# Kernel optimization log

Measured on AMD Instinct MI355X. Metric: run time of the kernel, lower is better.

The kernel has to match this reference:

```python
import jax, jax.numpy as jnp
import numpy as np

EPS = 1e-5
K = 3
N_TAP = K * K


def _bn(x, g, b, m, v):
    # eval-mode batchnorm over channel axis 1 of NCHW
    inv = g / jnp.sqrt(v + EPS)
    return x * inv[None, :, None, None] + (b - m * inv)[None, :, None, None]


def _silu(x):
    return x * jax.nn.sigmoid(x)


def _dcn(x, offset, mask, w, b, pad=1):
    """Modulated deformable conv (DCNv2), stride 1.
    x: [B,C,H,W], offset: [B,2n,H,W] ((dy,dx) per tap), mask: [B,n,H,W],
    w: [O,C,K,K], b: [O]."""
    B, C, H, W = x.shape
    O = w.shape[0]
    ky, kx = jnp.meshgrid(jnp.arange(K), jnp.arange(K), indexing='ij')
    ky = ky.reshape(N_TAP).astype(x.dtype)
    kx = kx.reshape(N_TAP).astype(x.dtype)
    off = offset.reshape(B, N_TAP, 2, H, W)
    base_y = jnp.arange(H, dtype=x.dtype)[None, None, :, None]
    base_x = jnp.arange(W, dtype=x.dtype)[None, None, None, :]
    # fractional sample positions [B,n,H,W]
    py = base_y - pad + ky[None, :, None, None] + off[:, :, 0]
    px = base_x - pad + kx[None, :, None, None] + off[:, :, 1]
    y0 = jnp.floor(py)
    x0 = jnp.floor(px)
    fy = py - y0
    fx = px - x0
    y0i = y0.astype(jnp.int32)
    x0i = x0.astype(jnp.int32)
    x_flat = x.reshape(B, C, 1, H * W)

    def corner(yi, xi, wgt):
        valid = (yi >= 0) & (yi < H) & (xi >= 0) & (xi < W)
        idx = (jnp.clip(yi, 0, H - 1) * W + jnp.clip(xi, 0, W - 1)).reshape(B, 1, N_TAP, H * W)
        v = jnp.take_along_axis(x_flat, idx, axis=-1)  # [B,C,n,HW]
        return v * (wgt * valid.astype(x.dtype)).reshape(B, 1, N_TAP, H * W)

    acc = corner(y0i, x0i, (1 - fy) * (1 - fx))
    acc = acc + corner(y0i, x0i + 1, (1 - fy) * fx)
    acc = acc + corner(y0i + 1, x0i, fy * (1 - fx))
    acc = acc + corner(y0i + 1, x0i + 1, fy * fx)
    val = acc.reshape(B, C, N_TAP, H, W) * mask[:, None]  # modulation
    out = jnp.einsum('bcnhw,ocn->bohw', val, w.reshape(O, C, N_TAP))
    return out + b[None, :, None, None]


def setup_inputs() -> dict:
    key = jax.random.key(0)
    ks = jax.random.split(key, 16)
    B, C1, H, W = 8, 256, 80, 80
    C2 = 256
    Ch = 128  # c_ = int(c2 * 0.5)
    d = {}
    d['x'] = jax.random.normal(ks[0], (B, C1, H, W), jnp.float32)
    # cv1: 1x1 conv (no bias) + BN
    d['cv1_w'] = jax.random.normal(ks[1], (Ch, C1), jnp.float32) * (1.0 / np.sqrt(C1))
    d['bn1_g'] = jax.random.uniform(ks[2], (Ch,), jnp.float32, 0.5, 1.5)
    d['bn1_b'] = jax.random.normal(ks[3], (Ch,), jnp.float32) * 0.1
    d['bn1_m'] = jax.random.normal(ks[4], (Ch,), jnp.float32) * 0.1
    d['bn1_v'] = jax.random.uniform(ks[5], (Ch,), jnp.float32, 0.5, 1.5)
    # offset/mask predictor 3x3 conv (small weights -> modest deformation)
    d['off_w'] = jax.random.normal(ks[6], (3 * N_TAP, Ch, K, K), jnp.float32) * 0.01
    d['off_b'] = jnp.zeros((3 * N_TAP,), jnp.float32)
    # dcn main weight/bias
    d['dcn_w'] = jax.random.normal(ks[7], (Ch, Ch, K, K), jnp.float32) * (1.0 / np.sqrt(Ch * N_TAP))
    d['dcn_b'] = jnp.zeros((Ch,), jnp.float32)
    d['bn2_g'] = jax.random.uniform(ks[8], (Ch,), jnp.float32, 0.5, 1.5)
    d['bn2_b'] = jax.random.normal(ks[9], (Ch,), jnp.float32) * 0.1
    d['bn2_m'] = jax.random.normal(ks[10], (Ch,), jnp.float32) * 0.1
    d['bn2_v'] = jax.random.uniform(ks[11], (Ch,), jnp.float32, 0.5, 1.5)
    # cv2: 1x1 conv (no bias) + BN
    d['cv2_w'] = jax.random.normal(ks[12], (C2, Ch), jnp.float32) * (1.0 / np.sqrt(Ch))
    d['bn3_g'] = jax.random.uniform(ks[13], (C2,), jnp.float32, 0.5, 1.5)
    d['bn3_b'] = jax.random.normal(ks[14], (C2,), jnp.float32) * 0.1
    d['bn3_m'] = jax.random.normal(ks[15], (C2,), jnp.float32) * 0.1
    d['bn3_v'] = jnp.ones((C2,), jnp.float32)
    return d


def reference(x, cv1_w, bn1_g, bn1_b, bn1_m, bn1_v,
              off_w, off_b, dcn_w, dcn_b, bn2_g, bn2_b, bn2_m, bn2_v,
              cv2_w, bn3_g, bn3_b, bn3_m, bn3_v):
    # cv1: 1x1 conv -> BN -> SiLU
    y = _silu(_bn(jnp.einsum('bchw,oc->bohw', x, cv1_w), bn1_g, bn1_b, bn1_m, bn1_v))
    # offset/mask predictor: 3x3 conv, pad 1
    raw = jax.lax.conv_general_dilated(
        y, off_w, window_strides=(1, 1), padding=((1, 1), (1, 1)),
        dimension_numbers=('NCHW', 'OIHW', 'NCHW')) + off_b[None, :, None, None]
    offset = raw[:, :2 * N_TAP]
    mask = jax.nn.sigmoid(raw[:, 2 * N_TAP:])
    # modulated deformable 3x3 conv -> BN -> SiLU
    y = _silu(_bn(_dcn(y, offset, mask, dcn_w, dcn_b), bn2_g, bn2_b, bn2_m, bn2_v))
    # cv2: 1x1 conv -> BN -> SiLU
    y = _silu(_bn(jnp.einsum('bchw,oc->bohw', y, cv2_w), bn3_g, bn3_b, bn3_m, bn3_v))
    return x + y  # shortcut (c1 == c2)
```

## Files before the change

kernel.cpp:

```cpp
#include <hip/hip_runtime.h>
#include <math.h>

#define HWSZ 6400
#define WIMG 80
#define HIMG 80
#define BEPS 1e-5f

typedef __attribute__((ext_vector_type(8))) short short8;
typedef __attribute__((ext_vector_type(4))) float f32x4;
typedef __attribute__((ext_vector_type(4))) unsigned u32x4;

__device__ __forceinline__ unsigned short f2b(float f) {
    unsigned u = __builtin_bit_cast(unsigned, f);
    u += 0x7fffu + ((u >> 16) & 1u);
    return (unsigned short)(u >> 16);
}
__device__ __forceinline__ float b2f(unsigned short h) {
    unsigned u = ((unsigned)h) << 16;
    return __builtin_bit_cast(float, u);
}
__device__ __forceinline__ float silu_f(float t) { return t / (1.f + __expf(-t)); }

__global__ __launch_bounds__(256) void k_prep(
    const float* __restrict__ cv1w, const float* __restrict__ g1, const float* __restrict__ b1,
    const float* __restrict__ m1, const float* __restrict__ v1,
    const float* __restrict__ offw, const float* __restrict__ offb,
    const float* __restrict__ dcnw, const float* __restrict__ dcnb,
    const float* __restrict__ g2, const float* __restrict__ b2,
    const float* __restrict__ m2, const float* __restrict__ v2,
    const float* __restrict__ cv2w, const float* __restrict__ g3, const float* __restrict__ b3,
    const float* __restrict__ m3, const float* __restrict__ v3,
    unsigned short* __restrict__ apk1, unsigned short* __restrict__ apko,
    unsigned short* __restrict__ apkd, unsigned short* __restrict__ apk2,
    float* __restrict__ bias1, float* __restrict__ biaso,
    float* __restrict__ bias2, float* __restrict__ bias3)
{
    int idx = blockIdx.x * 256 + threadIdx.x;
    if (idx < 32768) {
        int j = idx & 7, L = (idx >> 3) & 63, ks = (idx >> 9) & 7, mt = idx >> 12;
        int o = mt * 16 + (L & 15), k = ks * 32 + (L >> 4) * 8 + j;
        float inv = g1[o] * rsqrtf(v1[o] + BEPS);
        apk1[idx] = f2b(cv1w[o * 256 + k] * inv);
    } else if (idx < 69632) {
        int t = idx - 32768;
        int j = t & 7, L = (t >> 3) & 63;
        int mt = t / 18432, rem = t % 18432, ks = rem >> 9;
        int o = mt * 16 + (L & 15);
        int kp = ks * 32 + (L >> 4) * 8 + j;
        int n = kp >> 7, c = kp & 127;
        float wv = (o < 27) ? offw[(size_t)(o * 128 + c) * 9 + n] : 0.f;
        apko[t] = f2b(wv);
    } else if (idx < 217088) {
        int t = idx - 69632;
        int j = t & 7, L = (t >> 3) & 63;
        int mt = t / 18432, rem = t % 18432, ks = rem >> 9;
        int o = mt * 16 + (L & 15);
        int kp = ks * 32 + (L >> 4) * 8 + j;
        int n = kp >> 7, c = kp & 127;
        float inv = g2[o] * rsqrtf(v2[o] + BEPS);
        apkd[t] = f2b(dcnw[(size_t)(o * 128 + c) * 9 + n] * inv);
    } else if (idx < 249856) {
        int t = idx - 217088;
        int j = t & 7, L = (t >> 3) & 63, ks = (t >> 9) & 3, mt = t >> 11;
        int o = mt * 16 + (L & 15), k = ks * 32 + (L >> 4) * 8 + j;
        float inv = g3[o] * rsqrtf(v3[o] + BEPS);
        apk2[t] = f2b(cv2w[o * 128 + k] * inv);
    } else if (idx < 250395) {
        int t = idx - 249856;
        if (t < 128) { float inv = g1[t] * rsqrtf(v1[t] + BEPS); bias1[t] = b1[t] - m1[t] * inv; }
        else if (t < 155) { biaso[t - 128] = offb[t - 128]; }
        else if (t < 283) { int o = t - 155; float inv = g2[o] * rsqrtf(v2[o] + BEPS);
                            bias2[o] = dcnb[o] * inv + b2[o] - m2[o] * inv; }
        else { int o = t - 283; float inv = g3[o] * rsqrtf(v3[o] + BEPS); bias3[o] = b3[o] - m3[o] * inv; }
    }
}

__global__ __launch_bounds__(256) void k_cv1(
    const float* __restrict__ x, const unsigned short* __restrict__ apk1,
    const float* __restrict__ bias1, unsigned short* __restrict__ y1t)
{
    __shared__ __align__(16) unsigned short sB[20480];
    int blk = blockIdx.x;
    int b = blk / 100, pt = blk % 100;
    int p0 = pt * 64;
    int tid = threadIdx.x;
    int lane = tid & 63;
    int w = tid >> 6;
    {
        int px = lane, q = w;
        const float* xb = x + (size_t)b * 256 * HWSZ + p0 + px;
        for (int ks = 0; ks < 8; ++ks) {
            unsigned pk[4];
#pragma unroll
            for (int t = 0; t < 4; ++t) {
                float f0 = xb[(size_t)(ks * 32 + q * 8 + 2 * t) * HWSZ];
                float f1 = xb[(size_t)(ks * 32 + q * 8 + 2 * t + 1) * HWSZ];
                asm("v_cvt_pk_bf16_f32 %0, %1, %2" : "=v"(pk[t]) : "v"(f0), "v"(f1));
            }
            *(u32x4*)&sB[((ks * 4 + (px >> 4)) * 16 + (px & 15)) * 40 + q * 8] =
                (u32x4){pk[0], pk[1], pk[2], pk[3]};
        }
    }
    __syncthreads();
    int n16 = lane & 15, qd = lane >> 4;
    f32x4 acc[2][4];
#pragma unroll
    for (int mi = 0; mi < 2; ++mi)
#pragma unroll
        for (int nt = 0; nt < 4; ++nt) acc[mi][nt] = (f32x4){0.f, 0.f, 0.f, 0.f};
    for (int ks = 0; ks < 8; ++ks) {
        short8 bf[4];
#pragma unroll
        for (int nt = 0; nt < 4; ++nt)
            bf[nt] = *(const short8*)&sB[((ks * 4 + nt) * 16 + n16) * 40 + qd * 8];
#pragma unroll
        for (int mi = 0; mi < 2; ++mi) {
            int mt = w * 2 + mi;
            short8 af = *(const short8*)&apk1[(size_t)((mt * 8 + ks) * 64 + lane) * 8];
#pragma unroll
            for (int nt = 0; nt < 4; ++nt)
                acc[mi][nt] = __builtin_amdgcn_mfma_f32_16x16x32_bf16(af, bf[nt], acc[mi][nt], 0, 0, 0);
        }
    }
    __syncthreads();
#pragma unroll
    for (int mi = 0; mi < 2; ++mi)
#pragma unroll
        for (int nt = 0; nt < 4; ++nt)
#pragma unroll
            for (int r = 0; r < 4; ++r) {
                int o = w * 32 + mi * 16 + qd * 4 + r;
                float sv = silu_f(acc[mi][nt][r] + bias1[o]);
                sB[(nt * 16 + n16) * 136 + o] = f2b(sv);
            }
    __syncthreads();
    {
        int px = tid >> 2, qq = tid & 3;
        unsigned short* ytb = y1t + ((size_t)b * HWSZ + p0 + px) * 128;
#pragma unroll
        for (int seg = 0; seg < 4; ++seg) {
            short8 v = *(const short8*)&sB[px * 136 + qq * 32 + seg * 8];
            *(short8*)&ytb[qq * 32 + seg * 8] = v;
        }
    }
}

__global__ __launch_bounds__(256) void k_off(
    const unsigned short* __restrict__ y1t, const unsigned short* __restrict__ apko,
    const float* __restrict__ biaso, float* __restrict__ raw)
{
    __shared__ __align__(16) unsigned short sV[227 * 136];
    int blk = blockIdx.x;
    int b = blk / 100, pt = blk % 100;
    int p0 = pt * 64;
    int tid = threadIdx.x;
    const unsigned short* yb = y1t + (size_t)b * HWSZ * 128;
    for (int c = tid; c < 226 * 16; c += 256) {
        int row = c >> 4, col = c & 15;
        int sp = p0 - 81 + row;
        sp = min(max(sp, 0), HWSZ - 1);
        *(short8*)&sV[row * 136 + col * 8] = *(const short8*)&yb[(size_t)sp * 128 + col * 8];
    }
    if (tid < 16) {
        short8 z = {0, 0, 0, 0, 0, 0, 0, 0};
        *(short8*)&sV[226 * 136 + tid * 8] = z;
    }
    __syncthreads();

    int lane = tid & 63, w = tid >> 6;
    int n16 = lane & 15, qd = lane >> 4;
    int p = p0 + w * 16 + n16;
    int h = p / WIMG, wx = p % WIMG;
    f32x4 acc[2];
    acc[0] = (f32x4){0.f, 0.f, 0.f, 0.f};
    acc[1] = (f32x4){0.f, 0.f, 0.f, 0.f};
#pragma unroll
    for (int n = 0; n < 9; ++n) {
        int dh = n / 3 - 1, dw = n % 3 - 1;
        int hh = h + dh, ww = wx + dw;
        bool valid = ((unsigned)hh < HIMG) && ((unsigned)ww < WIMG);
        int row = valid ? (81 + w * 16 + n16 + dh * WIMG + dw) : 226;
        const unsigned short* rV = &sV[row * 136 + qd * 8];
#pragma unroll
        for (int s = 0; s < 4; ++s) {
            int ks = n * 4 + s;
            short8 bf = *(const short8*)&rV[s * 32];
#pragma unroll
            for (int mi = 0; mi < 2; ++mi) {
                short8 af = *(const short8*)&apko[(size_t)((mi * 36 + ks) * 64 + lane) * 8];
                acc[mi] = __builtin_amdgcn_mfma_f32_16x16x32_bf16(af, bf, acc[mi], 0, 0, 0);
            }
        }
    }
    float* rb = raw + (size_t)b * 27 * HWSZ + p0 + w * 16 + n16;
#pragma unroll
    for (int mi = 0; mi < 2; ++mi)
#pragma unroll
        for (int r = 0; r < 4; ++r) {
            int o = mi * 16 + qd * 4 + r;
            if (o < 27) {
                float t = acc[mi][r] + biaso[o];
                if (o >= 18) t = 1.f / (1.f + __expf(-t));
                rb[(size_t)o * HWSZ] = t;
            }
        }
}

#define HY 12
#define HX 12
#define NHALO 144

#define ACC8(uu, cb)                                                                   \
    {                                                                                  \
        _Pragma("unroll") for (int t = 0; t < 4; ++t) {                                \
            unsigned uv = (uu)[t];                                                     \
            av[(cb) + 2 * t] = fmaf(wk, __builtin_bit_cast(float, uv << 16),           \
                                    av[(cb) + 2 * t]);                                 \
            av[(cb) + 2 * t + 1] = fmaf(wk, __builtin_bit_cast(float, uv & 0xffff0000u),\
                                        av[(cb) + 2 * t + 1]);                         \
        }                                                                              \
    }

__global__ __launch_bounds__(256, 3) void k_dcn(
    const unsigned short* __restrict__ y1t, const float* __restrict__ raw,
    const unsigned short* __restrict__ apkd, const float* __restrict__ bias2,
    unsigned short* __restrict__ zt)
{
    __shared__ __align__(16) unsigned short sH[NHALO * 128];
    __shared__ float swy[2][9][64];
    __shared__ unsigned short sfx[9][64];
    __shared__ unsigned short sidx[4][9][64];

    int blk = blockIdx.x;
    int b = blk / 100, pt = blk % 100;
    int h0 = (pt / 10) * 8, w0 = (pt % 10) * 8;
    int tid = threadIdx.x;
    const unsigned short* yb = y1t + (size_t)b * HWSZ * 128;

    for (int i = tid; i < NHALO * 16; i += 256) {
        int r = i >> 4, u = i & 15;
        int ly = r / HX, lx = r % HX;
        int yy = min(max(h0 + ly - 2, 0), HIMG - 1);
        int xx = min(max(w0 + lx - 2, 0), WIMG - 1);
        *(u32x4*)&sH[r * 128 + (u ^ (r & 7)) * 8] =
            *(const u32x4*)&yb[(size_t)(yy * WIMG + xx) * 128 + u * 8];
    }
    for (int i = tid; i < 576; i += 256) {
        int n = i / 64, pp = i & 63;
        int h = h0 + (pp >> 3), wx = w0 + (pp & 7);
        int p = h * WIMG + wx;
        const float* rb = raw + (size_t)b * 27 * HWSZ + p;
        float dy = rb[(size_t)(2 * n) * HWSZ];
        float dx = rb[(size_t)(2 * n + 1) * HWSZ];
        float mk = rb[(size_t)(18 + n) * HWSZ];
        float py = (float)(h - 1 + n / 3) + dy;
        float px = (float)(wx - 1 + n % 3) + dx;
        float y0f = floorf(py), x0f = floorf(px);
        float fy = py - y0f, fx = px - x0f;
        int y0 = (int)y0f, x0 = (int)x0f;
        swy[0][n][pp] = (1.f - fy) * mk;
        swy[1][n][pp] = fy * mk;
        sfx[n][pp] = __builtin_bit_cast(unsigned short, (_Float16)fx);
#pragma unroll
        for (int k = 0; k < 4; ++k) {
            int yy = y0 + (k >> 1);
            int xx = x0 + (k & 1);
            unsigned valid = (((unsigned)yy < HIMG) && ((unsigned)xx < WIMG)) ? 0x8000u : 0u;
            int yc = min(max(yy, 0), HIMG - 1);
            int xc = min(max(xx, 0), WIMG - 1);
            sidx[k][n][pp] = (unsigned short)((yc << 7) | xc | valid);
        }
    }
    __syncthreads();

    int lane = tid & 63, w = tid >> 6;
    int n16 = lane & 15, qd = lane >> 4;
    int pxl = w * 16 + n16;
    f32x4 acc[8];
#pragma unroll
    for (int mt = 0; mt < 8; ++mt) acc[mt] = (f32x4){0.f, 0.f, 0.f, 0.f};

    for (int n = 0; n < 9; ++n) {
        float av[32];
#pragma unroll
        for (int j = 0; j < 32; ++j) av[j] = 0.f;
        float fxv = (float)__builtin_bit_cast(_Float16, sfx[n][pxl]);
        float fx1 = 1.f - fxv;
        float wy0 = swy[0][n][pxl], wy1 = swy[1][n][pxl];
#pragma unroll
        for (int k = 0; k < 4; ++k) {
            unsigned s = sidx[k][n][pxl];
            float wk = ((k >> 1) ? wy1 : wy0) * ((k & 1) ? fxv : fx1);
            if (!(s & 0x8000u)) wk = 0.f;
            int yc = (int)((s >> 7) & 127u), xc = (int)(s & 127u);
            int ly = yc - h0 + 2, lx = xc - w0 + 2;
            if (((unsigned)ly < HY) && ((unsigned)lx < HX)) {
                int r = ly * HX + lx;
                const unsigned short* hb = &sH[r * 128];
                int xr = r & 7;
                u32x4 u0 = *(const u32x4*)&hb[((qd) ^ xr) * 8];
                u32x4 u1 = *(const u32x4*)&hb[((4 + qd) ^ xr) * 8];
                u32x4 u2 = *(const u32x4*)&hb[((8 + qd) ^ xr) * 8];
                u32x4 u3 = *(const u32x4*)&hb[((12 + qd) ^ xr) * 8];
                ACC8(u0, 0) ACC8(u1, 8) ACC8(u2, 16) ACC8(u3, 24)
            } else if (wk != 0.f) {
                const unsigned short* src = &yb[(size_t)(yc * WIMG + xc) * 128 + qd * 8];
                u32x4 u0 = *(const u32x4*)src;
                u32x4 u1 = *(const u32x4*)(src + 32);
                u32x4 u2 = *(const u32x4*)(src + 64);
                u32x4 u3 = *(const u32x4*)(src + 96);
                ACC8(u0, 0) ACC8(u1, 8) ACC8(u2, 16) ACC8(u3, 24)
            }
        }
#pragma unroll
        for (int s = 0; s < 4; ++s) {
            unsigned pk[4];
#pragma unroll
            for (int t = 0; t < 4; ++t)
                asm("v_cvt_pk_bf16_f32 %0, %1, %2"
                    : "=v"(pk[t]) : "v"(av[s * 8 + 2 * t]), "v"(av[s * 8 + 2 * t + 1]));
            short8 bf = __builtin_bit_cast(short8, (u32x4){pk[0], pk[1], pk[2], pk[3]});
            int ks = n * 4 + s;
            const unsigned short* ap = apkd + (size_t)(ks * 64 + lane) * 8;
#pragma unroll
            for (int mt = 0; mt < 8; ++mt) {
                short8 af = *(const short8*)&ap[(size_t)mt * 18432];
                acc[mt] = __builtin_amdgcn_mfma_f32_16x16x32_bf16(af, bf, acc[mt], 0, 0, 0);
            }
        }
    }
    __syncthreads();
    unsigned short* sE = sH;
#pragma unroll
    for (int mt = 0; mt < 8; ++mt)
#pragma unroll
        for (int r = 0; r < 4; ++r) {
            int o = mt * 16 + qd * 4 + r;
            float sv = silu_f(acc[mt][r] + bias2[o]);
            sE[pxl * 136 + o] = f2b(sv);
        }
    __syncthreads();
    {
        int px = tid >> 2, qq = tid & 3;
        int p = (h0 + (px >> 3)) * WIMG + w0 + (px & 7);
        unsigned short* zb = zt + ((size_t)b * HWSZ + p) * 128;
#pragma unroll
        for (int seg = 0; seg < 4; ++seg) {
            short8 v = *(const short8*)&sE[px * 136 + qq * 32 + seg * 8];
            *(short8*)&zb[qq * 32 + seg * 8] = v;
        }
    }
}

__global__ __launch_bounds__(256) void k_cv2(
    const unsigned short* __restrict__ zt, const float* __restrict__ x,
    const unsigned short* __restrict__ apk2, const float* __restrict__ bias3,
    float* __restrict__ out)
{
    int blk = blockIdx.x;
    int b = blk / 100, pt = blk % 100;
    int p0 = pt * 64;
    int tid = threadIdx.x;
    int lane = tid & 63, w = tid >> 6;
    int n16 = lane & 15, qd = lane >> 4;
    const unsigned short* zb = zt + ((size_t)b * HWSZ + p0) * 128;
    f32x4 acc[4][4];
#pragma unroll
    for (int mi = 0; mi < 4; ++mi)
#pragma unroll
        for (int nt = 0; nt < 4; ++nt) acc[mi][nt] = (f32x4){0.f, 0.f, 0.f, 0.f};
#pragma unroll
    for (int ks = 0; ks < 4; ++ks) {
        short8 bf[4];
#pragma unroll
        for (int nt = 0; nt < 4; ++nt)
            bf[nt] = *(const short8*)&zb[(size_t)(nt * 16 + n16) * 128 + ks * 32 + qd * 8];
#pragma unroll
        for (int mi = 0; mi < 4; ++mi) {
            int mt = w * 4 + mi;
            short8 af = *(const short8*)&apk2[(size_t)((mt * 4 + ks) * 64 + lane) * 8];
#pragma unroll
            for (int nt = 0; nt < 4; ++nt)
                acc[mi][nt] = __builtin_amdgcn_mfma_f32_16x16x32_bf16(af, bf[nt], acc[mi][nt], 0, 0, 0);
        }
    }
    const float* xb = x + (size_t)b * 256 * HWSZ;
    float* ob = out + (size_t)b * 256 * HWSZ;
#pragma unroll
    for (int mi = 0; mi < 4; ++mi)
#pragma unroll
        for (int nt = 0; nt < 4; ++nt)
#pragma unroll
            for (int r = 0; r < 4; ++r) {
                int o = w * 64 + mi * 16 + qd * 4 + r;
                size_t idx = (size_t)o * HWSZ + p0 + nt * 16 + n16;
                ob[idx] = xb[idx] + silu_f(acc[mi][nt][r] + bias3[o]);
            }
}

extern "C" void kernel_launch(void* const* d_in, const int* in_sizes, int n_in,
                              void* d_out, int out_size, void* d_ws, size_t ws_size,
                              hipStream_t stream) {
    const float* x     = (const float*)d_in[0];
    const float* cv1w  = (const float*)d_in[1];
    const float* bn1g  = (const float*)d_in[2];
    const float* bn1b  = (const float*)d_in[3];
    const float* bn1m  = (const float*)d_in[4];
    const float* bn1v  = (const float*)d_in[5];
    const float* offw  = (const float*)d_in[6];
    const float* offb  = (const float*)d_in[7];
    const float* dcnw  = (const float*)d_in[8];
    const float* dcnb  = (const float*)d_in[9];
    const float* bn2g  = (const float*)d_in[10];
    const float* bn2b  = (const float*)d_in[11];
    const float* bn2m  = (const float*)d_in[12];
    const float* bn2v  = (const float*)d_in[13];
    const float* cv2w  = (const float*)d_in[14];
    const float* bn3g  = (const float*)d_in[15];
    const float* bn3b  = (const float*)d_in[16];
    const float* bn3m  = (const float*)d_in[17];
    const float* bn3v  = (const float*)d_in[18];
    float* out = (float*)d_out;

    float* base = (float*)d_ws;
    unsigned short* y1t = (unsigned short*)base;
    float* raw   = base + 3276800;
    unsigned short* zt  = (unsigned short*)(base + 4659200);
    unsigned short* apk1 = (unsigned short*)(base + 7936000);
    unsigned short* apko = (unsigned short*)(base + 7952384);
    unsigned short* apkd = (unsigned short*)(base + 7970816);
    unsigned short* apk2 = (unsigned short*)(base + 8044544);
    float* bias1 = base + 8060928;
    float* biaso = base + 8061056;
    float* bias2 = base + 8061088;
    float* bias3 = base + 8061216;

    k_prep<<<979, 256, 0, stream>>>(cv1w, bn1g, bn1b, bn1m, bn1v,
                                    offw, offb, dcnw, dcnb,
                                    bn2g, bn2b, bn2m, bn2v,
                                    cv2w, bn3g, bn3b, bn3m, bn3v,
                                    apk1, apko, apkd, apk2,
                                    bias1, biaso, bias2, bias3);
    k_cv1<<<800, 256, 0, stream>>>(x, apk1, bias1, y1t);
    k_off<<<800, 256, 0, stream>>>(y1t, apko, biaso, raw);
    k_dcn<<<800, 256, 0, stream>>>(y1t, raw, apkd, bias2, zt);
    k_cv2<<<800, 256, 0, stream>>>(zt, x, apk2, bias3, out);
}
```

Before: 245.8 us.

## Fuse offset conv, deformable conv and cv2 into one tiled kernel

Merges the offset-predictor conv, the deformable conv and the final 1x1 conv with residual into a single kernel working on 4x16 pixel tiles. The offset/mask values live in shared memory and the DCN output feeds cv2 directly, so the raw and zt round-trips through global memory and two launches go away. Weight packing is reordered so that all M-tiles for one K-step sit next to each other, and A-fragments are double-buffered across K-steps. The fused kernel holds more accumulators (16 f32x4 for cv2) and does extra halo work per tile, which may raise register pressure and lower occupancy.

```diff
diff --git a/kernel.cpp b/kernel.cpp
--- a/kernel.cpp
+++ b/kernel.cpp
@@ -15,11 +15,9 @@
     u += 0x7fffu + ((u >> 16) & 1u);
     return (unsigned short)(u >> 16);
 }
-__device__ __forceinline__ float b2f(unsigned short h) {
-    unsigned u = ((unsigned)h) << 16;
-    return __builtin_bit_cast(float, u);
-}
 __device__ __forceinline__ float silu_f(float t) { return t / (1.f + __expf(-t)); }
+
+#define BMFMA(a, b, c) __builtin_amdgcn_mfma_f32_16x16x32_bf16(a, b, c, 0, 0, 0)
 
 __global__ __launch_bounds__(256) void k_prep(
     const float* __restrict__ cv1w, const float* __restrict__ g1, const float* __restrict__ b1,
@@ -49,7 +47,7 @@
         int kp = ks * 32 + (L >> 4) * 8 + j;
         int n = kp >> 7, c = kp & 127;
         float wv = (o < 27) ? offw[(size_t)(o * 128 + c) * 9 + n] : 0.f;
-        apko[t] = f2b(wv);
+        apko[((size_t)(ks * 2 + mt) * 64 + L) * 8 + j] = f2b(wv);
     } else if (idx < 217088) {
         int t = idx - 69632;
         int j = t & 7, L = (t >> 3) & 63;
@@ -58,13 +56,13 @@
         int kp = ks * 32 + (L >> 4) * 8 + j;
         int n = kp >> 7, c = kp & 127;
         float inv = g2[o] * rsqrtf(v2[o] + BEPS);
-        apkd[t] = f2b(dcnw[(size_t)(o * 128 + c) * 9 + n] * inv);
+        apkd[((size_t)(ks * 8 + mt) * 64 + L) * 8 + j] = f2b(dcnw[(size_t)(o * 128 + c) * 9 + n] * inv);
     } else if (idx < 249856) {
         int t = idx - 217088;
         int j = t & 7, L = (t >> 3) & 63, ks = (t >> 9) & 3, mt = t >> 11;
         int o = mt * 16 + (L & 15), k = ks * 32 + (L >> 4) * 8 + j;
         float inv = g3[o] * rsqrtf(v3[o] + BEPS);
-        apk2[t] = f2b(cv2w[o * 128 + k] * inv);
+        apk2[((size_t)(ks * 16 + mt) * 64 + L) * 8 + j] = f2b(cv2w[o * 128 + k] * inv);
     } else if (idx < 250395) {
         int t = idx - 249856;
         if (t < 128) { float inv = g1[t] * rsqrtf(v1[t] + BEPS); bias1[t] = b1[t] - m1[t] * inv; }
@@ -113,14 +111,12 @@
 #pragma unroll
         for (int nt = 0; nt < 4; ++nt)
             bf[nt] = *(const short8*)&sB[((ks * 4 + nt) * 16 + n16) * 40 + qd * 8];
-#pragma unroll
-        for (int mi = 0; mi < 2; ++mi) {
-            int mt = w * 2 + mi;
-            short8 af = *(const short8*)&apk1[(size_t)((mt * 8 + ks) * 64 + lane) * 8];
-#pragma unroll
-            for (int nt = 0; nt < 4; ++nt)
-                acc[mi][nt] = __builtin_amdgcn_mfma_f32_16x16x32_bf16(af, bf[nt], acc[mi][nt], 0, 0, 0);
-        }
+        short8 a0 = *(const short8*)&apk1[(size_t)(((w * 2 + 0) * 8 + ks) * 64 + lane) * 8];
+        short8 a1 = *(const short8*)&apk1[(size_t)(((w * 2 + 1) * 8 + ks) * 64 + lane) * 8];
+#pragma unroll
+        for (int nt = 0; nt < 4; ++nt) acc[0][nt] = BMFMA(a0, bf[nt], acc[0][nt]);
+#pragma unroll
+        for (int nt = 0; nt < 4; ++nt) acc[1][nt] = BMFMA(a1, bf[nt], acc[1][nt]);
     }
     __syncthreads();
 #pragma unroll
@@ -145,70 +141,9 @@
     }
 }
 
-__global__ __launch_bounds__(256) void k_off(
-    const unsigned short* __restrict__ y1t, const unsigned short* __restrict__ apko,
-    const float* __restrict__ biaso, float* __restrict__ raw)
-{
-    __shared__ __align__(16) unsigned short sV[227 * 136];
-    int blk = blockIdx.x;
-    int b = blk / 100, pt = blk % 100;
-    int p0 = pt * 64;
-    int tid = threadIdx.x;
-    const unsigned short* yb = y1t + (size_t)b * HWSZ * 128;
-    for (int c = tid; c < 226 * 16; c += 256) {
-        int row = c >> 4, col = c & 15;
-        int sp = p0 - 81 + row;
-        sp = min(max(sp, 0), HWSZ - 1);
-        *(short8*)&sV[row * 136 + col * 8] = *(const short8*)&yb[(size_t)sp * 128 + col * 8];
-    }
-    if (tid < 16) {
-        short8 z = {0, 0, 0, 0, 0, 0, 0, 0};
-        *(short8*)&sV[226 * 136 + tid * 8] = z;
-    }
-    __syncthreads();
-
-    int lane = tid & 63, w = tid >> 6;
-    int n16 = lane & 15, qd = lane >> 4;
-    int p = p0 + w * 16 + n16;
-    int h = p / WIMG, wx = p % WIMG;
-    f32x4 acc[2];
-    acc[0] = (f32x4){0.f, 0.f, 0.f, 0.f};
-    acc[1] = (f32x4){0.f, 0.f, 0.f, 0.f};
-#pragma unroll
-    for (int n = 0; n < 9; ++n) {
-        int dh = n / 3 - 1, dw = n % 3 - 1;
-        int hh = h + dh, ww = wx + dw;
-        bool valid = ((unsigned)hh < HIMG) && ((unsigned)ww < WIMG);
-        int row = valid ? (81 + w * 16 + n16 + dh * WIMG + dw) : 226;
-        const unsigned short* rV = &sV[row * 136 + qd * 8];
-#pragma unroll
-        for (int s = 0; s < 4; ++s) {
-            int ks = n * 4 + s;
-            short8 bf = *(const short8*)&rV[s * 32];
-#pragma unroll
-            for (int mi = 0; mi < 2; ++mi) {
-                short8 af = *(const short8*)&apko[(size_t)((mi * 36 + ks) * 64 + lane) * 8];
-                acc[mi] = __builtin_amdgcn_mfma_f32_16x16x32_bf16(af, bf, acc[mi], 0, 0, 0);
-            }
-        }
-    }
-    float* rb = raw + (size_t)b * 27 * HWSZ + p0 + w * 16 + n16;
-#pragma unroll
-    for (int mi = 0; mi < 2; ++mi)
-#pragma unroll
-        for (int r = 0; r < 4; ++r) {
-            int o = mi * 16 + qd * 4 + r;
-            if (o < 27) {
-                float t = acc[mi][r] + biaso[o];
-                if (o >= 18) t = 1.f / (1.f + __expf(-t));
-                rb[(size_t)o * HWSZ] = t;
-            }
-        }
-}
-
-#define HY 12
-#define HX 12
-#define NHALO 144
+#define HY2 8
+#define HX2 20
+#define NH 160
 
 #define ACC8(uu, cb)                                                                   \
     {                                                                                  \
@@ -221,84 +156,125 @@
         }                                                                              \
     }
 
-__global__ __launch_bounds__(256, 3) void k_dcn(
-    const unsigned short* __restrict__ y1t, const float* __restrict__ raw,
+#define LDA8(dst, ksv)                                                                 \
+    _Pragma("unroll") for (int mt_ = 0; mt_ < 8; ++mt_)                                \
+        dst[mt_] = *(const short8*)&apkd[((size_t)((ksv) * 8 + mt_) * 64 + lane) * 8];
+
+#define MF8(afX, bfv)                                                                  \
+    _Pragma("unroll") for (int mt_ = 0; mt_ < 8; ++mt_)                                \
+        acc[mt_] = BMFMA(afX[mt_], bfv, acc[mt_]);
+
+#define PACKBF(bfv, sv)                                                                \
+    short8 bfv;                                                                        \
+    {                                                                                  \
+        unsigned pk0, pk1, pk2, pk3;                                                   \
+        asm("v_cvt_pk_bf16_f32 %0, %1, %2" : "=v"(pk0) : "v"(av[(sv)*8+0]), "v"(av[(sv)*8+1])); \
+        asm("v_cvt_pk_bf16_f32 %0, %1, %2" : "=v"(pk1) : "v"(av[(sv)*8+2]), "v"(av[(sv)*8+3])); \
+        asm("v_cvt_pk_bf16_f32 %0, %1, %2" : "=v"(pk2) : "v"(av[(sv)*8+4]), "v"(av[(sv)*8+5])); \
+        asm("v_cvt_pk_bf16_f32 %0, %1, %2" : "=v"(pk3) : "v"(av[(sv)*8+6]), "v"(av[(sv)*8+7])); \
+        bfv = __builtin_bit_cast(short8, (u32x4){pk0, pk1, pk2, pk3});                 \
+    }
+
+__global__ __launch_bounds__(256, 3) void k_odc(
+    const unsigned short* __restrict__ y1t,
+    const unsigned short* __restrict__ apko, const float* __restrict__ biaso,
     const unsigned short* __restrict__ apkd, const float* __restrict__ bias2,
-    unsigned short* __restrict__ zt)
+    const unsigned short* __restrict__ apk2, const float* __restrict__ bias3,
+    const float* __restrict__ x, float* __restrict__ out)
 {
-    __shared__ __align__(16) unsigned short sH[NHALO * 128];
-    __shared__ float swy[2][9][64];
-    __shared__ unsigned short sfx[9][64];
-    __shared__ unsigned short sidx[4][9][64];
+    __shared__ __align__(16) unsigned short sH[NH * 128];
+    __shared__ float sRaw[27 * 66];
 
     int blk = blockIdx.x;
     int b = blk / 100, pt = blk % 100;
-    int h0 = (pt / 10) * 8, w0 = (pt % 10) * 8;
-    int tid = threadIdx.x;
+    int h0 = (pt / 5) * 4, w0 = (pt % 5) * 16;
+    int tid = threadIdx.x, lane = tid & 63, w = tid >> 6;
+    int n16 = lane & 15, qd = lane >> 4;
+    int pxl = w * 16 + n16;
     const unsigned short* yb = y1t + (size_t)b * HWSZ * 128;
 
-    for (int i = tid; i < NHALO * 16; i += 256) {
+    for (int i = tid; i < NH * 16; i += 256) {
         int r = i >> 4, u = i & 15;
-        int ly = r / HX, lx = r % HX;
+        int ly = r / HX2, lx = r % HX2;
         int yy = min(max(h0 + ly - 2, 0), HIMG - 1);
         int xx = min(max(w0 + lx - 2, 0), WIMG - 1);
-        *(u32x4*)&sH[r * 128 + (u ^ (r & 7)) * 8] =
+        *(u32x4*)&sH[r * 128 + ((u ^ (r & 7)) * 8)] =
             *(const u32x4*)&yb[(size_t)(yy * WIMG + xx) * 128 + u * 8];
     }
-    for (int i = tid; i < 576; i += 256) {
-        int n = i / 64, pp = i & 63;
-        int h = h0 + (pp >> 3), wx = w0 + (pp & 7);
-        int p = h * WIMG + wx;
-        const float* rb = raw + (size_t)b * 27 * HWSZ + p;
-        float dy = rb[(size_t)(2 * n) * HWSZ];
-        float dx = rb[(size_t)(2 * n + 1) * HWSZ];
-        float mk = rb[(size_t)(18 + n) * HWSZ];
-        float py = (float)(h - 1 + n / 3) + dy;
-        float px = (float)(wx - 1 + n % 3) + dx;
+    __syncthreads();
+
+    {
+        f32x4 oa0 = (f32x4){0.f, 0.f, 0.f, 0.f};
+        f32x4 oa1 = (f32x4){0.f, 0.f, 0.f, 0.f};
+        for (int n = 0; n < 9; ++n) {
+            int dh = n / 3 - 1, dw = n % 3 - 1;
+            int hh = h0 + w + dh, ww = w0 + n16 + dw;
+            bool valid = ((unsigned)hh < HIMG) && ((unsigned)ww < WIMG);
+            int r = (w + 2 + dh) * HX2 + (n16 + 2 + dw);
+            int xr = r & 7;
+            const unsigned short* hb = &sH[r * 128];
+#pragma unroll
+            for (int s = 0; s < 4; ++s) {
+                short8 bf = *(const short8*)&hb[((s * 4 + qd) ^ xr) * 8];
+                if (!valid) bf = (short8){0, 0, 0, 0, 0, 0, 0, 0};
+                int ks = n * 4 + s;
+                short8 a0 = *(const short8*)&apko[((size_t)(ks * 2 + 0) * 64 + lane) * 8];
+                short8 a1 = *(const short8*)&apko[((size_t)(ks * 2 + 1) * 64 + lane) * 8];
+                oa0 = BMFMA(a0, bf, oa0);
+                oa1 = BMFMA(a1, bf, oa1);
+            }
+        }
+#pragma unroll
+        for (int mi = 0; mi < 2; ++mi)
+#pragma unroll
+            for (int r4 = 0; r4 < 4; ++r4) {
+                int o = mi * 16 + qd * 4 + r4;
+                if (o < 27) {
+                    float t = (mi ? oa1[r4] : oa0[r4]) + biaso[o];
+                    if (o >= 18) t = 1.f / (1.f + __expf(-t));
+                    sRaw[o * 66 + pxl] = t;
+                }
+            }
+    }
+    __syncthreads();
+
+    f32x4 acc[8];
+#pragma unroll
+    for (int mt = 0; mt < 8; ++mt) acc[mt] = (f32x4){0.f, 0.f, 0.f, 0.f};
+    int hI = h0 + w, wI = w0 + n16;
+
+    for (int n = 0; n < 9; ++n) {
+        float dy = sRaw[(2 * n) * 66 + pxl];
+        float dx = sRaw[(2 * n + 1) * 66 + pxl];
+        float mk = sRaw[(18 + n) * 66 + pxl];
+        float py = (float)(hI - 1 + n / 3) + dy;
+        float px = (float)(wI - 1 + n % 3) + dx;
         float y0f = floorf(py), x0f = floorf(px);
-        float fy = py - y0f, fx = px - x0f;
+        float fy = py - y0f, fxv = px - x0f;
         int y0 = (int)y0f, x0 = (int)x0f;
-        swy[0][n][pp] = (1.f - fy) * mk;
-        swy[1][n][pp] = fy * mk;
-        sfx[n][pp] = __builtin_bit_cast(unsigned short, (_Float16)fx);
+        float wy0 = (1.f - fy) * mk, wy1 = fy * mk, fx1 = 1.f - fxv;
+
+        int ks0 = n * 4;
+        short8 afA[8], afB[8];
+        LDA8(afA, ks0)
+
+        float av[32];
+#pragma unroll
+        for (int j = 0; j < 32; ++j) av[j] = 0.f;
 #pragma unroll
         for (int k = 0; k < 4; ++k) {
-            int yy = y0 + (k >> 1);
-            int xx = x0 + (k & 1);
-            unsigned valid = (((unsigned)yy < HIMG) && ((unsigned)xx < WIMG)) ? 0x8000u : 0u;
+            int yy = y0 + (k >> 1), xx = x0 + (k & 1);
+            bool vld = ((unsigned)yy < HIMG) && ((unsigned)xx < WIMG);
+            float wk = ((k >> 1) ? wy1 : wy0) * ((k & 1) ? fxv : fx1);
+            if (!vld) wk = 0.f;
             int yc = min(max(yy, 0), HIMG - 1);
             int xc = min(max(xx, 0), WIMG - 1);
-            sidx[k][n][pp] = (unsigned short)((yc << 7) | xc | valid);
-        }
-    }
-    __syncthreads();
-
-    int lane = tid & 63, w = tid >> 6;
-    int n16 = lane & 15, qd = lane >> 4;
-    int pxl = w * 16 + n16;
-    f32x4 acc[8];
-#pragma unroll
-    for (int mt = 0; mt < 8; ++mt) acc[mt] = (f32x4){0.f, 0.f, 0.f, 0.f};
-
-    for (int n = 0; n < 9; ++n) {
-        float av[32];
-#pragma unroll
-        for (int j = 0; j < 32; ++j) av[j] = 0.f;
-        float fxv = (float)__builtin_bit_cast(_Float16, sfx[n][pxl]);
-        float fx1 = 1.f - fxv;
-        float wy0 = swy[0][n][pxl], wy1 = swy[1][n][pxl];
-#pragma unroll
-        for (int k = 0; k < 4; ++k) {
-            unsigned s = sidx[k][n][pxl];
-            float wk = ((k >> 1) ? wy1 : wy0) * ((k & 1) ? fxv : fx1);
-            if (!(s & 0x8000u)) wk = 0.f;
-            int yc = (int)((s >> 7) & 127u), xc = (int)(s & 127u);
             int ly = yc - h0 + 2, lx = xc - w0 + 2;
-            if (((unsigned)ly < HY) && ((unsigned)lx < HX)) {
-                int r = ly * HX + lx;
+            if (((unsigned)ly < HY2) && ((unsigned)lx < HX2)) {
+                int r = ly * HX2 + lx;
                 const unsigned short* hb = &sH[r * 128];
                 int xr = r & 7;
-                u32x4 u0 = *(const u32x4*)&hb[((qd) ^ xr) * 8];
+                u32x4 u0 = *(const u32x4*)&hb[((0 + qd) ^ xr) * 8];
                 u32x4 u1 = *(const u32x4*)&hb[((4 + qd) ^ xr) * 8];
                 u32x4 u2 = *(const u32x4*)&hb[((8 + qd) ^ xr) * 8];
                 u32x4 u3 = *(const u32x4*)&hb[((12 + qd) ^ xr) * 8];
@@ -312,90 +288,56 @@
                 ACC8(u0, 0) ACC8(u1, 8) ACC8(u2, 16) ACC8(u3, 24)
             }
         }
-#pragma unroll
-        for (int s = 0; s < 4; ++s) {
-            unsigned pk[4];
-#pragma unroll
-            for (int t = 0; t < 4; ++t)
-                asm("v_cvt_pk_bf16_f32 %0, %1, %2"
-                    : "=v"(pk[t]) : "v"(av[s * 8 + 2 * t]), "v"(av[s * 8 + 2 * t + 1]));
-            short8 bf = __builtin_bit_cast(short8, (u32x4){pk[0], pk[1], pk[2], pk[3]});
-            int ks = n * 4 + s;
-            const unsigned short* ap = apkd + (size_t)(ks * 64 + lane) * 8;
-#pragma unroll
-            for (int mt = 0; mt < 8; ++mt) {
-                short8 af = *(const short8*)&ap[(size_t)mt * 18432];
-                acc[mt] = __builtin_amdgcn_mfma_f32_16x16x32_bf16(af, bf, acc[mt], 0, 0, 0);
-            }
-        }
-    }
-    __syncthreads();
+        LDA8(afB, ks0 + 1)
+        { PACKBF(bf0, 0) MF8(afA, bf0) }
+        LDA8(afA, ks0 + 2)
+        { PACKBF(bf1, 1) MF8(afB, bf1) }
+        LDA8(afB, ks0 + 3)
+        { PACKBF(bf2, 2) MF8(afA, bf2) }
+        { PACKBF(bf3, 3) MF8(afB, bf3) }
+    }
+    __syncthreads();
+
     unsigned short* sE = sH;
 #pragma unroll
     for (int mt = 0; mt < 8; ++mt)
 #pragma unroll
-        for (int r = 0; r < 4; ++r) {
-            int o = mt * 16 + qd * 4 + r;
-            float sv = silu_f(acc[mt][r] + bias2[o]);
+        for (int r4 = 0; r4 < 4; ++r4) {
+            int o = mt * 16 + qd * 4 + r4;
+            float sv = silu_f(acc[mt][r4] + bias2[o]);
             sE[pxl * 136 + o] = f2b(sv);
         }
     __syncthreads();
-    {
-        int px = tid >> 2, qq = tid & 3;
-        int p = (h0 + (px >> 3)) * WIMG + w0 + (px & 7);
-        unsigned short* zb = zt + ((size_t)b * HWSZ + p) * 128;
-#pragma unroll
-        for (int seg = 0; seg < 4; ++seg) {
-            short8 v = *(const short8*)&sE[px * 136 + qq * 32 + seg * 8];
-            *(short8*)&zb[qq * 32 + seg * 8] = v;
-        }
-    }
-}
-
-__global__ __launch_bounds__(256) void k_cv2(
-    const unsigned short* __restrict__ zt, const float* __restrict__ x,
-    const unsigned short* __restrict__ apk2, const float* __restrict__ bias3,
-    float* __restrict__ out)
-{
-    int blk = blockIdx.x;
-    int b = blk / 100, pt = blk % 100;
-    int p0 = pt * 64;
-    int tid = threadIdx.x;
-    int lane = tid & 63, w = tid >> 6;
-    int n16 = lane & 15, qd = lane >> 4;
-    const unsigned short* zb = zt + ((size_t)b * HWSZ + p0) * 128;
-    f32x4 acc[4][4];
-#pragma unroll
-    for (int mi = 0; mi < 4; ++mi)
-#pragma unroll
-        for (int nt = 0; nt < 4; ++nt) acc[mi][nt] = (f32x4){0.f, 0.f, 0.f, 0.f};
+
+    f32x4 c2[16];
+#pragma unroll
+    for (int mt = 0; mt < 16; ++mt) c2[mt] = (f32x4){0.f, 0.f, 0.f, 0.f};
 #pragma unroll
     for (int ks = 0; ks < 4; ++ks) {
-        short8 bf[4];
-#pragma unroll
-        for (int nt = 0; nt < 4; ++nt)
-            bf[nt] = *(const short8*)&zb[(size_t)(nt * 16 + n16) * 128 + ks * 32 + qd * 8];
-#pragma unroll
-        for (int mi = 0; mi < 4; ++mi) {
-            int mt = w * 4 + mi;
-            short8 af = *(const short8*)&apk2[(size_t)((mt * 4 + ks) * 64 + lane) * 8];
-#pragma unroll
-            for (int nt = 0; nt < 4; ++nt)
-                acc[mi][nt] = __builtin_amdgcn_mfma_f32_16x16x32_bf16(af, bf[nt], acc[mi][nt], 0, 0, 0);
-        }
-    }
+        short8 bf = *(const short8*)&sE[pxl * 136 + ks * 32 + qd * 8];
+        short8 cfA[8], cfB[8];
+#pragma unroll
+        for (int mt_ = 0; mt_ < 8; ++mt_)
+            cfA[mt_] = *(const short8*)&apk2[((size_t)(ks * 16 + mt_) * 64 + lane) * 8];
+#pragma unroll
+        for (int mt_ = 0; mt_ < 8; ++mt_)
+            cfB[mt_] = *(const short8*)&apk2[((size_t)(ks * 16 + 8 + mt_) * 64 + lane) * 8];
+#pragma unroll
+        for (int mt_ = 0; mt_ < 8; ++mt_) c2[mt_] = BMFMA(cfA[mt_], bf, c2[mt_]);
+#pragma unroll
+        for (int mt_ = 0; mt_ < 8; ++mt_) c2[8 + mt_] = BMFMA(cfB[mt_], bf, c2[8 + mt_]);
+    }
+    int p = (h0 + w) * WIMG + w0 + n16;
     const float* xb = x + (size_t)b * 256 * HWSZ;
     float* ob = out + (size_t)b * 256 * HWSZ;
 #pragma unroll
-    for (int mi = 0; mi < 4; ++mi)
-#pragma unroll
-        for (int nt = 0; nt < 4; ++nt)
-#pragma unroll
-            for (int r = 0; r < 4; ++r) {
-                int o = w * 64 + mi * 16 + qd * 4 + r;
-                size_t idx = (size_t)o * HWSZ + p0 + nt * 16 + n16;
-                ob[idx] = xb[idx] + silu_f(acc[mi][nt][r] + bias3[o]);
-            }
+    for (int mt = 0; mt < 16; ++mt)
+#pragma unroll
+        for (int r4 = 0; r4 < 4; ++r4) {
+            int o = mt * 16 + qd * 4 + r4;
+            size_t idx = (size_t)o * HWSZ + p;
+            ob[idx] = xb[idx] + silu_f(c2[mt][r4] + bias3[o]);
+        }
 }
 
 extern "C" void kernel_launch(void* const* d_in, const int* in_sizes, int n_in,
@@ -424,8 +366,6 @@
 
     float* base = (float*)d_ws;
     unsigned short* y1t = (unsigned short*)base;
-    float* raw   = base + 3276800;
-    unsigned short* zt  = (unsigned short*)(base + 4659200);
     unsigned short* apk1 = (unsigned short*)(base + 7936000);
     unsigned short* apko = (unsigned short*)(base + 7952384);
     unsigned short* apkd = (unsigned short*)(base + 7970816);
@@ -442,7 +382,6 @@
                                     apk1, apko, apkd, apk2,
                                     bias1, biaso, bias2, bias3);
     k_cv1<<<800, 256, 0, stream>>>(x, apk1, bias1, y1t);
-    k_off<<<800, 256, 0, stream>>>(y1t, apko, biaso, raw);
-    k_dcn<<<800, 256, 0, stream>>>(y1t, raw, apkd, bias2, zt);
-    k_cv2<<<800, 256, 0, stream>>>(zt, x, apk2, bias3, out);
-}
+    k_odc<<<800, 256, 0, stream>>>(y1t, apko, biaso, apkd, bias2,
+                                   apk2, bias3, x, out);
+}
```

Result: no change. 245.5 us (-0.1%).
